# Kernel tuning notes

Hardware: AMD Instinct MI355X
Metric: run time of the kernel (lower is better)

## Reference

```python
import jax, jax.numpy as jnp
import numpy as np

B, T, S, D, V, NX = 4, 256, 400, 512, 50000, 50
VEXT = V + NX  # extended vocab


def setup_inputs() -> dict:
    key = jax.random.key(0)
    ks = jax.random.split(key, 10)
    s = 0.02
    return {
        "x": jax.random.normal(ks[0], (B, T, D), dtype=jnp.float32),
        "enc_outputs": jax.random.normal(ks[1], (B, S, D), dtype=jnp.float32),
        "src_mask": jax.random.randint(ks[2], (B, 1, S), 0, 2, dtype=jnp.int32),
        "enc_batch_extend_vocab": jax.random.randint(ks[3], (B, S), 0, VEXT, dtype=jnp.int64),
        "extra_zeros": jnp.zeros((B, T, NX), dtype=jnp.float32),
        "fc_w": jax.random.normal(ks[4], (V, D), dtype=jnp.float32) * s,
        "fc_b": jnp.zeros((V,), dtype=jnp.float32),
        "pgen_w": jax.random.normal(ks[5], (1, D), dtype=jnp.float32) * s,
        "pgen_b": jnp.zeros((1,), dtype=jnp.float32),
        "wq": jax.random.normal(ks[6], (D, D), dtype=jnp.float32) * s,
        "bq": jnp.zeros((D,), dtype=jnp.float32),
        "wk": jax.random.normal(ks[7], (D, D), dtype=jnp.float32) * s,
        "bk": jnp.zeros((D,), dtype=jnp.float32),
    }


def reference(x, enc_outputs, src_mask, enc_batch_extend_vocab, extra_zeros,
              fc_w, fc_b, pgen_w, pgen_b, wq, bq, wk, bk):
    # vocab distribution: [B,T,V]
    p_vocab = jax.nn.softmax(x @ fc_w.T + fc_b, axis=-1)
    # single-head cross attention probs (h=1 -> d_k = D)
    q = x @ wq.T + bq                 # [B,T,D]
    k = enc_outputs @ wk.T + bk       # [B,S,D]
    scores = jnp.einsum('btd,bsd->bts', q, k) / jnp.sqrt(jnp.float32(D))
    scores = jnp.where(src_mask == 0, jnp.float32(-1e9), scores)  # mask [B,1,S]
    attn_probs = jax.nn.softmax(scores, axis=-1)  # [B,T,S]
    # generation gate
    p_gen = jax.nn.sigmoid(x @ pgen_w.T + pgen_b)  # [B,T,1]
    attn_dist = (1.0 - p_gen) * attn_probs         # copy distribution over source
    p_ext = jnp.concatenate([p_gen * p_vocab, extra_zeros], axis=-1)  # [B,T,VEXT]
    # scatter-add copy probs into extended vocab slots
    b_idx = jnp.arange(B)[:, None, None]
    t_idx = jnp.arange(T)[None, :, None]
    v_idx = enc_batch_extend_vocab[:, None, :]
    bb, tt, vv = jnp.broadcast_arrays(b_idx, t_idx, v_idx)  # each [B,T,S]
    p_ext = p_ext.at[bb, tt, vv].add(attn_dist)
    return jnp.log(jnp.maximum(p_ext, jnp.float32(1e-9)))
```

## Files before the change

### kernel.cpp

```cpp
#include <hip/hip_runtime.h>
#include <hip/hip_bf16.h>
#include <math.h>

constexpr int cB = 4, cT = 256, cS = 400, cD = 512, cV = 50000, cNX = 50;
constexpr int cVEXT = cV + cNX;
constexpr int cPAN  = (cV + 127) / 128;
constexpr int cCBLD = cVEXT * 2;
constexpr int cTOP  = 50100;
constexpr int cMQ   = cB * cT;

typedef __attribute__((ext_vector_type(8))) short short8v;
typedef __attribute__((ext_vector_type(4))) float floatx4;

__device__ inline ushort f2bf(float f) {
    union { float f; unsigned u; } v; v.f = f;
    unsigned r = (v.u + 0x7FFFu + ((v.u >> 16) & 1u)) >> 16;
    return (ushort)r;
}
__device__ inline float bf2f(ushort u) {
    union { unsigned u; float f; } v; v.u = ((unsigned)u) << 16;
    return v.f;
}

__global__ __launch_bounds__(256) void cast_kernel(
    const float* __restrict__ src, ushort* __restrict__ dst, int n4)
{
    const int stride = gridDim.x * 256;
    for (int i = blockIdx.x * 256 + threadIdx.x; i < n4; i += stride) {
        float4 v = *(const float4*)(src + (size_t)i * 4);
        ushort4 o;
        o.x = f2bf(v.x); o.y = f2bf(v.y); o.z = f2bf(v.z); o.w = f2bf(v.w);
        *(ushort4*)(dst + (size_t)i * 4) = o;
    }
}

template<bool STATS>
__global__ __launch_bounds__(256) void gemm2(
    const ushort* __restrict__ A, const ushort* __restrict__ Wb,
    const float* __restrict__ bias,
    float* __restrict__ Cf, ushort* __restrict__ Cb,
    float* __restrict__ pm, float* __restrict__ ps,
    int M, int N, int K, int ldc)
{
    __shared__ ushort As[2][128 * 32];
    __shared__ ushort Bs[2][128 * 32];
    __shared__ float sm_m[2][128];
    __shared__ float sm_s[2][128];

    const int tid  = threadIdx.x;
    const int lane = tid & 63;
    const int wv   = tid >> 6;
    const int wm   = wv >> 1;
    const int wn   = wv & 1;

    int bm, bn, pan = 0;
    if constexpr (STATS) {
        const int wg  = blockIdx.y * gridDim.x + blockIdx.x;
        const int nwg = gridDim.x * gridDim.y;
        const int j   = (wg & 7) * (nwg >> 3) + (wg >> 3);
        pan = j >> 3;
        bm  = (j & 7) * 128;
        bn  = pan * 128;
    } else {
        bm = blockIdx.x * 128;
        bn = blockIdx.y * 128;
    }

    const int rA = lane & 15;
    const int kA = (lane >> 4) * 8;
    const int nt = K >> 5;

    floatx4 acc[4][4] = {};

    auto stage = [&](int bidx, int t) {
        const int k0 = t * 32;
        #pragma unroll
        for (int c = 0; c < 2; ++c) {
            const int chunk = wv * 2 + c;
            int ga = bm + chunk * 16 + rA; if (ga >= M) ga = M - 1;
            __builtin_amdgcn_global_load_lds(
                (const __attribute__((address_space(1))) void*)(A + (size_t)ga * K + k0 + kA),
                (__attribute__((address_space(3))) void*)&As[bidx][chunk * 512], 16, 0, 0);
            int gb = bn + chunk * 16 + rA; if (gb >= N) gb = N - 1;
            __builtin_amdgcn_global_load_lds(
                (const __attribute__((address_space(1))) void*)(Wb + (size_t)gb * K + k0 + kA),
                (__attribute__((address_space(3))) void*)&Bs[bidx][chunk * 512], 16, 0, 0);
        }
    };

    stage(0, 0);
    __syncthreads();

    const int fr = lane & 15;
    const int g  = lane >> 4;
    int buf = 0;

    for (int t = 0; t < nt; ++t) {
        if (t + 1 < nt) stage(buf ^ 1, t + 1);
        short8v a[4], b[4];
        #pragma unroll
        for (int mi = 0; mi < 4; ++mi)
            a[mi] = *(const short8v*)&As[buf][(wm * 4 + mi) * 512 + lane * 8];
        #pragma unroll
        for (int ni = 0; ni < 4; ++ni)
            b[ni] = *(const short8v*)&Bs[buf][(wn * 4 + ni) * 512 + lane * 8];
        #pragma unroll
        for (int mi = 0; mi < 4; ++mi)
            #pragma unroll
            for (int ni = 0; ni < 4; ++ni)
                acc[mi][ni] = __builtin_amdgcn_mfma_f32_16x16x32_bf16(
                    a[mi], b[ni], acc[mi][ni], 0, 0, 0);
        __syncthreads();
        buf ^= 1;
    }

    float bv[4]; bool val[4];
    #pragma unroll
    for (int ni = 0; ni < 4; ++ni) {
        const int colg = bn + wn * 64 + ni * 16 + fr;
        val[ni] = (colg < N);
        bv[ni] = val[ni] ? bias[colg] : 0.f;
    }
    #pragma unroll
    for (int mi = 0; mi < 4; ++mi)
        #pragma unroll
        for (int ni = 0; ni < 4; ++ni)
            #pragma unroll
            for (int r = 0; r < 4; ++r)
                acc[mi][ni][r] += bv[ni];

    if constexpr (STATS) {
        #pragma unroll
        for (int mi = 0; mi < 4; ++mi) {
            #pragma unroll
            for (int r = 0; r < 4; ++r) {
                float mx = -1e30f;
                #pragma unroll
                for (int ni = 0; ni < 4; ++ni)
                    if (val[ni]) mx = fmaxf(mx, acc[mi][ni][r]);
                #pragma unroll
                for (int sw = 1; sw < 16; sw <<= 1)
                    mx = fmaxf(mx, __shfl_xor(mx, sw));
                float sm = 0.f;
                #pragma unroll
                for (int ni = 0; ni < 4; ++ni)
                    if (val[ni]) sm += __expf(acc[mi][ni][r] - mx);
                #pragma unroll
                for (int sw = 1; sw < 16; sw <<= 1)
                    sm += __shfl_xor(sm, sw);
                if (fr == 0) {
                    const int rl = wm * 64 + mi * 16 + g * 4 + r;
                    sm_m[wn][rl] = mx;
                    sm_s[wn][rl] = sm;
                }
            }
        }
        __syncthreads();
        if (tid < 128) {
            const float m0 = sm_m[0][tid], m1 = sm_m[1][tid];
            const float s0 = sm_s[0][tid], s1 = sm_s[1][tid];
            const float mm = fmaxf(m0, m1);
            const float ss = s0 * __expf(m0 - mm) + s1 * __expf(m1 - mm);
            const int grow = bm + tid;
            if (grow < M) {
                pm[(size_t)pan * M + grow] = mm;
                ps[(size_t)pan * M + grow] = ss;
            }
        }
        #pragma unroll
        for (int mi = 0; mi < 4; ++mi) {
            #pragma unroll
            for (int ni = 0; ni < 4; ++ni) {
                if (!val[ni]) continue;
                const int colg = bn + wn * 64 + ni * 16 + fr;
                #pragma unroll
                for (int r = 0; r < 4; ++r) {
                    const int row = bm + wm * 64 + mi * 16 + g * 4 + r;
                    Cb[(size_t)row * cCBLD + cTOP + colg] = f2bf(acc[mi][ni][r]);
                }
            }
        }
    } else {
        #pragma unroll
        for (int mi = 0; mi < 4; ++mi) {
            #pragma unroll
            for (int ni = 0; ni < 4; ++ni) {
                if (!val[ni]) continue;
                const int colg = bn + wn * 64 + ni * 16 + fr;
                #pragma unroll
                for (int r = 0; r < 4; ++r) {
                    const int row = bm + wm * 64 + mi * 16 + g * 4 + r;
                    if (row < M) Cf[(size_t)row * ldc + colg] = acc[mi][ni][r];
                }
            }
        }
    }
}

__global__ __launch_bounds__(256) void combine_kernel(
    const float* __restrict__ pm, const float* __restrict__ ps,
    const float* __restrict__ pgen, float* __restrict__ rowadd)
{
    const int lane = threadIdx.x & 63;
    const int wv   = threadIdx.x >> 6;
    const int row  = blockIdx.x * 64 + lane;

    float m = -1e30f, s = 0.f;
    #pragma unroll 2
    for (int i = wv; i < cPAN; i += 4) {
        const float mi = pm[(size_t)i * cMQ + row];
        const float si = ps[(size_t)i * cMQ + row];
        const float nm = fmaxf(m, mi);
        s = s * __expf(m - nm) + si * __expf(mi - nm);
        m = nm;
    }
    __shared__ float rm[4][64], rs[4][64];
    rm[wv][lane] = m; rs[wv][lane] = s;
    __syncthreads();
    if (wv == 0) {
        m = rm[0][lane]; s = rs[0][lane];
        #pragma unroll
        for (int i = 1; i < 4; ++i) {
            const float m2 = rm[i][lane], s2 = rs[i][lane];
            const float nm = fmaxf(m, m2);
            s = s * __expf(m - nm) + s2 * __expf(m2 - nm);
            m = nm;
        }
        rowadd[row] = __logf(pgen[row]) - m - __logf(s);
    }
}

__global__ __launch_bounds__(512) void transform_reg(
    float* __restrict__ out, const float* __restrict__ rowadd,
    const int* __restrict__ ebev, const float* __restrict__ attn)
{
    const int row = blockIdx.x;
    const int b   = row / cT;
    const int tid = threadIdx.x;
    constexpr float LOGMIN = -20.72326583694641f;

    __shared__ int   pos[cS];
    __shared__ float add[cS];
    for (int s = tid; s < cS; s += 512) {
        pos[s] = ebev[b * cS + s];
        add[s] = attn[(size_t)row * cS + s];
    }

    const float a = rowadd[row];
    const ushort* rowu = (const ushort*)out + (size_t)row * cCBLD + cTOP;
    float* rowf = out + (size_t)row * cVEXT;

    #pragma unroll 1
    for (int t = 0; t < 13; ++t) {
        const int cidx = t * 512 + tid;
        const bool v = cidx < cV / 8;
        ushort4 lo = {}, hi = {};
        if (v) {
            lo = *(const ushort4*)(rowu + (size_t)cidx * 8);
            hi = *(const ushort4*)(rowu + (size_t)cidx * 8 + 4);
        }
        __syncthreads();
        if (v) {
            const int j = cidx * 8;
            float2 o;
            o.x = fmaxf(bf2f(lo.x) + a, LOGMIN);
            o.y = fmaxf(bf2f(lo.y) + a, LOGMIN);
            *(float2*)(rowf + j) = o;
            o.x = fmaxf(bf2f(lo.z) + a, LOGMIN);
            o.y = fmaxf(bf2f(lo.w) + a, LOGMIN);
            *(float2*)(rowf + j + 2) = o;
            o.x = fmaxf(bf2f(hi.x) + a, LOGMIN);
            o.y = fmaxf(bf2f(hi.y) + a, LOGMIN);
            *(float2*)(rowf + j + 4) = o;
            o.x = fmaxf(bf2f(hi.z) + a, LOGMIN);
            o.y = fmaxf(bf2f(hi.w) + a, LOGMIN);
            *(float2*)(rowf + j + 6) = o;
        }
    }
    if (tid < (cVEXT - cV) / 2) {
        float2 z; z.x = LOGMIN; z.y = LOGMIN;
        *(float2*)(rowf + cV + 2 * tid) = z;
    }
    __syncthreads();

    for (int s = tid; s < cS; s += 512) {
        const int p = pos[s];
        bool leader = true;
        for (int s2 = 0; s2 < s; ++s2)
            if (pos[s2] == p) { leader = false; break; }
        if (!leader) continue;
        float sum = add[s];
        for (int s2 = s + 1; s2 < cS; ++s2)
            if (pos[s2] == p) sum += add[s2];
        const float base = __expf(rowf[p]);
        rowf[p] = __logf(fmaxf(base + sum, 1e-9f));
    }
}

__global__ __launch_bounds__(64) void pgen_kernel(
    const float* __restrict__ x, const float* __restrict__ w,
    const float* __restrict__ b, float* __restrict__ pgen)
{
    const int row = blockIdx.x;
    const int lane = threadIdx.x;
    const float* xr = x + (size_t)row * cD;
    float s = 0.f;
    for (int i = lane; i < cD; i += 64) s += xr[i] * w[i];
    #pragma unroll
    for (int off = 32; off; off >>= 1) s += __shfl_down(s, off);
    if (lane == 0) pgen[row] = 1.f / (1.f + __expf(-(s + b[0])));
}

__global__ __launch_bounds__(256) void attn_kernel(
    const float* __restrict__ q, const float* __restrict__ k,
    const int* __restrict__ src_mask, const float* __restrict__ pgen,
    float* __restrict__ attn)
{
    constexpr float scale = 0.04419417382415922f;
    const int row = blockIdx.x;
    const int b = row / cT;
    const int tid = threadIdx.x;

    __shared__ __align__(16) float qs[cD];
    __shared__ float sc[cS];
    __shared__ float red[4];

    for (int i = tid; i < cD; i += 256) qs[i] = q[(size_t)row * cD + i];
    __syncthreads();

    for (int s = tid; s < cS; s += 256) {
        const float* kr = k + ((size_t)b * cS + s) * cD;
        float dot = 0.f;
        #pragma unroll 4
        for (int i = 0; i < cD; i += 4) {
            float4 kv = *(const float4*)(kr + i);
            float4 qv = *(const float4*)(qs + i);
            dot += qv.x * kv.x + qv.y * kv.y + qv.z * kv.z + qv.w * kv.w;
        }
        float v = dot * scale;
        if (src_mask[b * cS + s] == 0) v = -1e9f;
        sc[s] = v;
    }
    __syncthreads();

    float m = -3.4e38f;
    for (int s = tid; s < cS; s += 256) m = fmaxf(m, sc[s]);
    #pragma unroll
    for (int off = 32; off; off >>= 1) m = fmaxf(m, __shfl_down(m, off));
    if ((tid & 63) == 0) red[tid >> 6] = m;
    __syncthreads();
    m = fmaxf(fmaxf(red[0], red[1]), fmaxf(red[2], red[3]));
    __syncthreads();

    float sum = 0.f;
    for (int s = tid; s < cS; s += 256) {
        float e = __expf(sc[s] - m);
        sc[s] = e;
        sum += e;
    }
    #pragma unroll
    for (int off = 32; off; off >>= 1) sum += __shfl_down(sum, off);
    if ((tid & 63) == 0) red[tid >> 6] = sum;
    __syncthreads();
    sum = red[0] + red[1] + red[2] + red[3];

    const float w = (1.f - pgen[row]) / sum;
    for (int s = tid; s < cS; s += 256)
        attn[(size_t)row * cS + s] = sc[s] * w;
}

extern "C" void kernel_launch(void* const* d_in, const int* in_sizes, int n_in,
                              void* d_out, int out_size, void* d_ws, size_t ws_size,
                              hipStream_t stream)
{
    const float* x      = (const float*)d_in[0];
    const float* enc    = (const float*)d_in[1];
    const int*   mask   = (const int*)d_in[2];
    const int*   ebev   = (const int*)d_in[3];
    const float* fc_w   = (const float*)d_in[5];
    const float* fc_b   = (const float*)d_in[6];
    const float* pgen_w = (const float*)d_in[7];
    const float* pgen_b = (const float*)d_in[8];
    const float* wq     = (const float*)d_in[9];
    const float* bq     = (const float*)d_in[10];
    const float* wk     = (const float*)d_in[11];
    const float* bk     = (const float*)d_in[12];
    float* out = (float*)d_out;

    float* ws     = (float*)d_ws;
    float* q      = ws;
    float* kbuf   = q + (size_t)cB * cT * cD;
    float* pgen   = kbuf + (size_t)cB * cS * cD;
    float* attn   = pgen + cB * cT;
    float* pm     = attn + (size_t)cB * cT * cS;
    float* ps     = pm + (size_t)cPAN * cMQ;
    float* rowadd = ps + (size_t)cPAN * cMQ;
    ushort* xb    = (ushort*)(rowadd + cMQ);
    ushort* encb  = xb + (size_t)cB * cT * cD;
    ushort* wqb   = encb + (size_t)cB * cS * cD;
    ushort* wkb   = wqb + (size_t)cD * cD;
    ushort* wb    = wkb + (size_t)cD * cD;

    const dim3 blk(256);
    const int MQ = cMQ;
    const int MK = cB * cS;

    cast_kernel<<<dim3(512), blk, 0, stream>>>(x, xb, (cB * cT * cD) / 4);
    cast_kernel<<<dim3(512), blk, 0, stream>>>(enc, encb, (cB * cS * cD) / 4);
    cast_kernel<<<dim3(256), blk, 0, stream>>>(wq, wqb, (cD * cD) / 4);
    cast_kernel<<<dim3(256), blk, 0, stream>>>(wk, wkb, (cD * cD) / 4);
    cast_kernel<<<dim3(2048), blk, 0, stream>>>(fc_w, wb, (cV * cD) / 4);

    gemm2<false><<<dim3(MQ / 128, cD / 128), blk, 0, stream>>>(
        xb, wqb, bq, q, nullptr, nullptr, nullptr, MQ, cD, cD, cD);
    gemm2<false><<<dim3((MK + 127) / 128, cD / 128), blk, 0, stream>>>(
        encb, wkb, bk, kbuf, nullptr, nullptr, nullptr, MK, cD, cD, cD);
    pgen_kernel<<<dim3(MQ), dim3(64), 0, stream>>>(x, pgen_w, pgen_b, pgen);

    attn_kernel<<<dim3(MQ), blk, 0, stream>>>(q, kbuf, mask, pgen, attn);

    gemm2<true><<<dim3(8, cPAN), blk, 0, stream>>>(
        xb, wb, fc_b, nullptr, (ushort*)out, pm, ps, MQ, cV, cD, 0);

    combine_kernel<<<dim3(MQ / 64), blk, 0, stream>>>(pm, ps, pgen, rowadd);

    transform_reg<<<dim3(MQ), dim3(512), 0, stream>>>(out, rowadd, ebev, attn);
}
```

Before: 443.5 us.

## Widen vocab GEMM tile to 128x256 with 8 waves; batch transform loads

Splits the templated GEMM into a small projection kernel and a dedicated vocab GEMM that uses 512 threads and a 128x256 output tile, so each staged A tile is reused across twice as many vocab columns. This halves the number of panels and the per-panel softmax statistics the combine kernel reduces. The transform kernel now issues all 13 bf16 loads into registers before a single barrier, instead of a barrier per iteration. The costs are more registers per thread in the transform kernel and larger LDS use per block in the vocab GEMM, which may lower occupancy.

```diff
diff --git a/kernel.cpp b/kernel.cpp
--- a/kernel.cpp
+++ b/kernel.cpp
@@ -4,7 +4,7 @@
 
 constexpr int cB = 4, cT = 256, cS = 400, cD = 512, cV = 50000, cNX = 50;
 constexpr int cVEXT = cV + cNX;
-constexpr int cPAN  = (cV + 127) / 128;
+constexpr int cPAN2 = (cV + 255) / 256;
 constexpr int cCBLD = cVEXT * 2;
 constexpr int cTOP  = 50100;
 constexpr int cMQ   = cB * cT;
@@ -34,37 +34,21 @@
     }
 }
 
-template<bool STATS>
-__global__ __launch_bounds__(256) void gemm2(
+__global__ __launch_bounds__(256) void gemm_proj(
     const ushort* __restrict__ A, const ushort* __restrict__ Wb,
-    const float* __restrict__ bias,
-    float* __restrict__ Cf, ushort* __restrict__ Cb,
-    float* __restrict__ pm, float* __restrict__ ps,
+    const float* __restrict__ bias, float* __restrict__ Cf,
     int M, int N, int K, int ldc)
 {
     __shared__ ushort As[2][128 * 32];
     __shared__ ushort Bs[2][128 * 32];
-    __shared__ float sm_m[2][128];
-    __shared__ float sm_s[2][128];
 
     const int tid  = threadIdx.x;
     const int lane = tid & 63;
     const int wv   = tid >> 6;
     const int wm   = wv >> 1;
     const int wn   = wv & 1;
-
-    int bm, bn, pan = 0;
-    if constexpr (STATS) {
-        const int wg  = blockIdx.y * gridDim.x + blockIdx.x;
-        const int nwg = gridDim.x * gridDim.y;
-        const int j   = (wg & 7) * (nwg >> 3) + (wg >> 3);
-        pan = j >> 3;
-        bm  = (j & 7) * 128;
-        bn  = pan * 128;
-    } else {
-        bm = blockIdx.x * 128;
-        bn = blockIdx.y * 128;
-    }
+    const int bm   = blockIdx.x * 128;
+    const int bn   = blockIdx.y * 128;
 
     const int rA = lane & 15;
     const int kA = (lane >> 4) * 8;
@@ -91,10 +75,7 @@
     stage(0, 0);
     __syncthreads();
 
-    const int fr = lane & 15;
-    const int g  = lane >> 4;
     int buf = 0;
-
     for (int t = 0; t < nt; ++t) {
         if (t + 1 < nt) stage(buf ^ 1, t + 1);
         short8v a[4], b[4];
@@ -114,11 +95,102 @@
         buf ^= 1;
     }
 
+    const int fr = lane & 15;
+    const int g  = lane >> 4;
+    #pragma unroll
+    for (int mi = 0; mi < 4; ++mi) {
+        #pragma unroll
+        for (int ni = 0; ni < 4; ++ni) {
+            const int colg = bn + wn * 64 + ni * 16 + fr;
+            if (colg >= N) continue;
+            const float bv = bias[colg];
+            #pragma unroll
+            for (int r = 0; r < 4; ++r) {
+                const int row = bm + wm * 64 + mi * 16 + g * 4 + r;
+                if (row < M) Cf[(size_t)row * ldc + colg] = acc[mi][ni][r] + bv;
+            }
+        }
+    }
+}
+
+__global__ __launch_bounds__(512) void gemm_big(
+    const ushort* __restrict__ A, const ushort* __restrict__ Wb,
+    const float* __restrict__ bias, ushort* __restrict__ Cb,
+    float* __restrict__ pm, float* __restrict__ ps)
+{
+    __shared__ ushort As[2][8 * 512];
+    __shared__ ushort Bs[2][16 * 512];
+    __shared__ float sm_m[4][128];
+    __shared__ float sm_s[4][128];
+
+    const int tid  = threadIdx.x;
+    const int lane = tid & 63;
+    const int wv   = tid >> 6;
+    const int wm   = wv >> 2;
+    const int wn   = wv & 3;
+
+    const int wg  = blockIdx.y * gridDim.x + blockIdx.x;
+    const int nwg = gridDim.x * gridDim.y;
+    const int j   = (wg & 7) * (nwg >> 3) + (wg >> 3);
+    const int pan = j >> 3;
+    const int bm  = (j & 7) * 128;
+    const int bn  = pan * 256;
+
+    const int rA = lane & 15;
+    const int kA = (lane >> 4) * 8;
+
+    floatx4 acc[4][4] = {};
+
+    auto stage = [&](int bidx, int t) {
+        const int k0 = t * 32;
+        {
+            const int ga = bm + wv * 16 + rA;
+            __builtin_amdgcn_global_load_lds(
+                (const __attribute__((address_space(1))) void*)(A + (size_t)ga * cD + k0 + kA),
+                (__attribute__((address_space(3))) void*)&As[bidx][wv * 512], 16, 0, 0);
+        }
+        #pragma unroll
+        for (int c = 0; c < 2; ++c) {
+            const int chunk = wv * 2 + c;
+            int gb = bn + chunk * 16 + rA; if (gb >= cV) gb = cV - 1;
+            __builtin_amdgcn_global_load_lds(
+                (const __attribute__((address_space(1))) void*)(Wb + (size_t)gb * cD + k0 + kA),
+                (__attribute__((address_space(3))) void*)&Bs[bidx][chunk * 512], 16, 0, 0);
+        }
+    };
+
+    stage(0, 0);
+    __syncthreads();
+
+    int buf = 0;
+    #pragma unroll 1
+    for (int t = 0; t < 16; ++t) {
+        if (t + 1 < 16) stage(buf ^ 1, t + 1);
+        short8v a[4], b[4];
+        #pragma unroll
+        for (int mi = 0; mi < 4; ++mi)
+            a[mi] = *(const short8v*)&As[buf][(wm * 4 + mi) * 512 + lane * 8];
+        #pragma unroll
+        for (int ni = 0; ni < 4; ++ni)
+            b[ni] = *(const short8v*)&Bs[buf][(wn * 4 + ni) * 512 + lane * 8];
+        #pragma unroll
+        for (int mi = 0; mi < 4; ++mi)
+            #pragma unroll
+            for (int ni = 0; ni < 4; ++ni)
+                acc[mi][ni] = __builtin_amdgcn_mfma_f32_16x16x32_bf16(
+                    a[mi], b[ni], acc[mi][ni], 0, 0, 0);
+        __syncthreads();
+        buf ^= 1;
+    }
+
+    const int fr = lane & 15;
+    const int g  = lane >> 4;
+
     float bv[4]; bool val[4];
     #pragma unroll
     for (int ni = 0; ni < 4; ++ni) {
         const int colg = bn + wn * 64 + ni * 16 + fr;
-        val[ni] = (colg < N);
+        val[ni] = (colg < cV);
         bv[ni] = val[ni] ? bias[colg] : 0.f;
     }
     #pragma unroll
@@ -129,69 +201,56 @@
             for (int r = 0; r < 4; ++r)
                 acc[mi][ni][r] += bv[ni];
 
-    if constexpr (STATS) {
-        #pragma unroll
-        for (int mi = 0; mi < 4; ++mi) {
+    #pragma unroll
+    for (int mi = 0; mi < 4; ++mi) {
+        #pragma unroll
+        for (int r = 0; r < 4; ++r) {
+            float mx = -1e30f;
+            #pragma unroll
+            for (int ni = 0; ni < 4; ++ni)
+                if (val[ni]) mx = fmaxf(mx, acc[mi][ni][r]);
+            #pragma unroll
+            for (int sw = 1; sw < 16; sw <<= 1)
+                mx = fmaxf(mx, __shfl_xor(mx, sw));
+            float sm = 0.f;
+            #pragma unroll
+            for (int ni = 0; ni < 4; ++ni)
+                if (val[ni]) sm += __expf(acc[mi][ni][r] - mx);
+            #pragma unroll
+            for (int sw = 1; sw < 16; sw <<= 1)
+                sm += __shfl_xor(sm, sw);
+            if (fr == 0) {
+                const int rl = wm * 64 + mi * 16 + g * 4 + r;
+                sm_m[wn][rl] = mx;
+                sm_s[wn][rl] = sm;
+            }
+        }
+    }
+    __syncthreads();
+    if (tid < 128) {
+        float m = sm_m[0][tid], s = sm_s[0][tid];
+        #pragma unroll
+        for (int i = 1; i < 4; ++i) {
+            const float m2 = sm_m[i][tid], s2 = sm_s[i][tid];
+            const float nm = fmaxf(m, m2);
+            s = s * __expf(m - nm) + s2 * __expf(m2 - nm);
+            m = nm;
+        }
+        const int grow = bm + tid;
+        pm[(size_t)pan * cMQ + grow] = m;
+        ps[(size_t)pan * cMQ + grow] = s;
+    }
+
+    #pragma unroll
+    for (int mi = 0; mi < 4; ++mi) {
+        #pragma unroll
+        for (int ni = 0; ni < 4; ++ni) {
+            if (!val[ni]) continue;
+            const int colg = bn + wn * 64 + ni * 16 + fr;
             #pragma unroll
             for (int r = 0; r < 4; ++r) {
-                float mx = -1e30f;
-                #pragma unroll
-                for (int ni = 0; ni < 4; ++ni)
-                    if (val[ni]) mx = fmaxf(mx, acc[mi][ni][r]);
-                #pragma unroll
-                for (int sw = 1; sw < 16; sw <<= 1)
-                    mx = fmaxf(mx, __shfl_xor(mx, sw));
-                float sm = 0.f;
-                #pragma unroll
-                for (int ni = 0; ni < 4; ++ni)
-                    if (val[ni]) sm += __expf(acc[mi][ni][r] - mx);
-                #pragma unroll
-                for (int sw = 1; sw < 16; sw <<= 1)
-                    sm += __shfl_xor(sm, sw);
-                if (fr == 0) {
-                    const int rl = wm * 64 + mi * 16 + g * 4 + r;
-                    sm_m[wn][rl] = mx;
-                    sm_s[wn][rl] = sm;
-                }
-            }
-        }
-        __syncthreads();
-        if (tid < 128) {
-            const float m0 = sm_m[0][tid], m1 = sm_m[1][tid];
-            const float s0 = sm_s[0][tid], s1 = sm_s[1][tid];
-            const float mm = fmaxf(m0, m1);
-            const float ss = s0 * __expf(m0 - mm) + s1 * __expf(m1 - mm);
-            const int grow = bm + tid;
-            if (grow < M) {
-                pm[(size_t)pan * M + grow] = mm;
-                ps[(size_t)pan * M + grow] = ss;
-            }
-        }
-        #pragma unroll
-        for (int mi = 0; mi < 4; ++mi) {
-            #pragma unroll
-            for (int ni = 0; ni < 4; ++ni) {
-                if (!val[ni]) continue;
-                const int colg = bn + wn * 64 + ni * 16 + fr;
-                #pragma unroll
-                for (int r = 0; r < 4; ++r) {
-                    const int row = bm + wm * 64 + mi * 16 + g * 4 + r;
-                    Cb[(size_t)row * cCBLD + cTOP + colg] = f2bf(acc[mi][ni][r]);
-                }
-            }
-        }
-    } else {
-        #pragma unroll
-        for (int mi = 0; mi < 4; ++mi) {
-            #pragma unroll
-            for (int ni = 0; ni < 4; ++ni) {
-                if (!val[ni]) continue;
-                const int colg = bn + wn * 64 + ni * 16 + fr;
-                #pragma unroll
-                for (int r = 0; r < 4; ++r) {
-                    const int row = bm + wm * 64 + mi * 16 + g * 4 + r;
-                    if (row < M) Cf[(size_t)row * ldc + colg] = acc[mi][ni][r];
-                }
+                const int row = bm + wm * 64 + mi * 16 + g * 4 + r;
+                Cb[(size_t)row * cCBLD + cTOP + colg] = f2bf(acc[mi][ni][r]);
             }
         }
     }
@@ -207,7 +266,7 @@
 
     float m = -1e30f, s = 0.f;
     #pragma unroll 2
-    for (int i = wv; i < cPAN; i += 4) {
+    for (int i = wv; i < cPAN2; i += 4) {
         const float mi = pm[(size_t)i * cMQ + row];
         const float si = ps[(size_t)i * cMQ + row];
         const float nm = fmaxf(m, mi);
@@ -238,6 +297,7 @@
     const int b   = row / cT;
     const int tid = threadIdx.x;
     constexpr float LOGMIN = -20.72326583694641f;
+    constexpr int NCHUNK = cV / 8;
 
     __shared__ int   pos[cS];
     __shared__ float add[cS];
@@ -250,31 +310,35 @@
     const ushort* rowu = (const ushort*)out + (size_t)row * cCBLD + cTOP;
     float* rowf = out + (size_t)row * cVEXT;
 
-    #pragma unroll 1
+    ushort4 lo[13], hi[13];
+    #pragma unroll
     for (int t = 0; t < 13; ++t) {
         const int cidx = t * 512 + tid;
-        const bool v = cidx < cV / 8;
-        ushort4 lo = {}, hi = {};
-        if (v) {
-            lo = *(const ushort4*)(rowu + (size_t)cidx * 8);
-            hi = *(const ushort4*)(rowu + (size_t)cidx * 8 + 4);
-        }
-        __syncthreads();
-        if (v) {
-            const int j = cidx * 8;
+        if (cidx < NCHUNK) {
+            lo[t] = *(const ushort4*)(rowu + (size_t)cidx * 8);
+            hi[t] = *(const ushort4*)(rowu + (size_t)cidx * 8 + 4);
+        }
+    }
+    __syncthreads();
+
+    #pragma unroll
+    for (int t = 0; t < 13; ++t) {
+        const int cidx = t * 512 + tid;
+        if (cidx < NCHUNK) {
+            const int jb = cidx * 8;
             float2 o;
-            o.x = fmaxf(bf2f(lo.x) + a, LOGMIN);
-            o.y = fmaxf(bf2f(lo.y) + a, LOGMIN);
-            *(float2*)(rowf + j) = o;
-            o.x = fmaxf(bf2f(lo.z) + a, LOGMIN);
-            o.y = fmaxf(bf2f(lo.w) + a, LOGMIN);
-            *(float2*)(rowf + j + 2) = o;
-            o.x = fmaxf(bf2f(hi.x) + a, LOGMIN);
-            o.y = fmaxf(bf2f(hi.y) + a, LOGMIN);
-            *(float2*)(rowf + j + 4) = o;
-            o.x = fmaxf(bf2f(hi.z) + a, LOGMIN);
-            o.y = fmaxf(bf2f(hi.w) + a, LOGMIN);
-            *(float2*)(rowf + j + 6) = o;
+            o.x = fmaxf(bf2f(lo[t].x) + a, LOGMIN);
+            o.y = fmaxf(bf2f(lo[t].y) + a, LOGMIN);
+            *(float2*)(rowf + jb) = o;
+            o.x = fmaxf(bf2f(lo[t].z) + a, LOGMIN);
+            o.y = fmaxf(bf2f(lo[t].w) + a, LOGMIN);
+            *(float2*)(rowf + jb + 2) = o;
+            o.x = fmaxf(bf2f(hi[t].x) + a, LOGMIN);
+            o.y = fmaxf(bf2f(hi[t].y) + a, LOGMIN);
+            *(float2*)(rowf + jb + 4) = o;
+            o.x = fmaxf(bf2f(hi[t].z) + a, LOGMIN);
+            o.y = fmaxf(bf2f(hi[t].w) + a, LOGMIN);
+            *(float2*)(rowf + jb + 6) = o;
         }
     }
     if (tid < (cVEXT - cV) / 2) {
@@ -393,8 +457,8 @@
     float* pgen   = kbuf + (size_t)cB * cS * cD;
     float* attn   = pgen + cB * cT;
     float* pm     = attn + (size_t)cB * cT * cS;
-    float* ps     = pm + (size_t)cPAN * cMQ;
-    float* rowadd = ps + (size_t)cPAN * cMQ;
+    float* ps     = pm + (size_t)cPAN2 * cMQ;
+    float* rowadd = ps + (size_t)cPAN2 * cMQ;
     ushort* xb    = (ushort*)(rowadd + cMQ);
     ushort* encb  = xb + (size_t)cB * cT * cD;
     ushort* wqb   = encb + (size_t)cB * cS * cD;
@@ -411,16 +475,16 @@
     cast_kernel<<<dim3(256), blk, 0, stream>>>(wk, wkb, (cD * cD) / 4);
     cast_kernel<<<dim3(2048), blk, 0, stream>>>(fc_w, wb, (cV * cD) / 4);
 
-    gemm2<false><<<dim3(MQ / 128, cD / 128), blk, 0, stream>>>(
-        xb, wqb, bq, q, nullptr, nullptr, nullptr, MQ, cD, cD, cD);
-    gemm2<false><<<dim3((MK + 127) / 128, cD / 128), blk, 0, stream>>>(
-        encb, wkb, bk, kbuf, nullptr, nullptr, nullptr, MK, cD, cD, cD);
+    gemm_proj<<<dim3(MQ / 128, cD / 128), blk, 0, stream>>>(
+        xb, wqb, bq, q, MQ, cD, cD, cD);
+    gemm_proj<<<dim3((MK + 127) / 128, cD / 128), blk, 0, stream>>>(
+        encb, wkb, bk, kbuf, MK, cD, cD, cD);
     pgen_kernel<<<dim3(MQ), dim3(64), 0, stream>>>(x, pgen_w, pgen_b, pgen);
 
     attn_kernel<<<dim3(MQ), blk, 0, stream>>>(q, kbuf, mask, pgen, attn);
 
-    gemm2<true><<<dim3(8, cPAN), blk, 0, stream>>>(
-        xb, wb, fc_b, nullptr, (ushort*)out, pm, ps, MQ, cV, cD, 0);
+    gemm_big<<<dim3(8, cPAN2), dim3(512), 0, stream>>>(
+        xb, wb, fc_b, (ushort*)out, pm, ps);
 
     combine_kernel<<<dim3(MQ / 64), blk, 0, stream>>>(pm, ps, pgen, rowadd);
 
```

After: 423.3 us. 4.6% less time.
